# Optimization experiments

Measured on AMD Instinct MI355X. Metric: run time of the kernel, lower is better.

## Reference

```python
import math
import jax, jax.numpy as jnp
import numpy as np

INIT_TEMPERATURE = 0.07
MAX_SCALE = 100.0
B, D = 16384, 256


def setup_inputs() -> dict:
    key = jax.random.key(0)
    k1, k2 = jax.random.split(key)
    z_schema = jax.random.normal(k1, (B, D), dtype=jnp.float32)
    z_seal = jax.random.normal(k2, (B, D), dtype=jnp.float32)
    logit_scale = jnp.asarray(math.log(1.0 / INIT_TEMPERATURE), dtype=jnp.float32)
    return {"z_schema": z_schema, "z_seal": z_seal, "logit_scale": logit_scale}


def reference(z_schema, z_seal, logit_scale):
    # scale = min(exp(logit_scale), max_scale)
    scale = jnp.minimum(jnp.exp(logit_scale), jnp.float32(MAX_SCALE))
    # logits[i, j] = <z_schema[i], z_seal[j]> * scale   (B, B)
    logits = jnp.einsum("id,jd->ij", z_schema, z_seal) * scale
    # cross-entropy with labels = arange(B): loss = mean(lse(row) - diag)
    diag = jnp.diagonal(logits)
    lse_rows = jax.nn.logsumexp(logits, axis=1)  # s2r direction
    lse_cols = jax.nn.logsumexp(logits, axis=0)  # r2s direction (logits.T rows)
    loss_s2r = jnp.mean(lse_rows - diag)
    loss_r2s = jnp.mean(lse_cols - diag)
    loss = (loss_s2r + loss_r2s) * 0.5
    return (loss, loss)
```

## Files before the change

kernel.cpp:

```cpp
#include <hip/hip_runtime.h>
#include <hip/hip_bf16.h>
#include <math.h>

#define B_N 16384
#define D_K 256
#define JS 8
#define JRANGE (B_N / JS)
#define TJ 32
#define NT (JRANGE / TJ)
#define TILE_BYTES (TJ * D_K * 2)

typedef __bf16 bf16x8 __attribute__((ext_vector_type(8)));
typedef float f32x16 __attribute__((ext_vector_type(16)));

__device__ __forceinline__ unsigned short f2bf(float x) {
  unsigned u = __float_as_uint(x);
  unsigned r = (u + 0x7fffu + ((u >> 16) & 1u)) >> 16;
  return (unsigned short)r;
}

__device__ __forceinline__ float fexp2(float x) {
#if __has_builtin(__builtin_amdgcn_exp2f)
  return __builtin_amdgcn_exp2f(x);
#else
  return exp2f(x);
#endif
}

__device__ __forceinline__ void load_lds16(const void* g, void* l) {
  __builtin_amdgcn_global_load_lds(
      (const __attribute__((address_space(1))) unsigned int*)g,
      (__attribute__((address_space(3))) unsigned int*)l, 16, 0, 0);
}

__global__ void convert_kernel(const float* __restrict__ A, const float* __restrict__ Bm,
                               const float* __restrict__ lsp,
                               unsigned short* __restrict__ Abf,
                               unsigned short* __restrict__ Bbf) {
  const float c = fminf(expf(lsp[0]), 100.0f) * 1.4426950408889634f;
  int idx = (blockIdx.x * blockDim.x + threadIdx.x) * 4;
  float4 a = *(const float4*)(A + idx);
  float4 b = *(const float4*)(Bm + idx);
  ushort4 ua, ub;
  ua.x = f2bf(a.x); ua.y = f2bf(a.y); ua.z = f2bf(a.z); ua.w = f2bf(a.w);
  ub.x = f2bf(b.x * c); ub.y = f2bf(b.y * c); ub.z = f2bf(b.z * c); ub.w = f2bf(b.w * c);
  *(ushort4*)(Abf + idx) = ua;
  *(ushort4*)(Bbf + idx) = ub;
}

__global__ void diag_kernel(const float* __restrict__ A, const float* __restrict__ Bm,
                            float* __restrict__ diag) {
  int w = threadIdx.x >> 6, l = threadIdx.x & 63;
  int row = blockIdx.x * 4 + w;
  const float4* a = (const float4*)(A + row * D_K);
  const float4* b = (const float4*)(Bm + row * D_K);
  float4 av = a[l], bv = b[l];
  float s = av.x * bv.x + av.y * bv.y + av.z * bv.z + av.w * bv.w;
#pragma unroll
  for (int off = 32; off; off >>= 1) s += __shfl_xor(s, off);
  if (l == 0) diag[row] = s;
}

__device__ __forceinline__ void upd(float& m, float& s, const f32x16& a) {
  float t = a[0];
#pragma unroll
  for (int r = 1; r < 16; ++r) t = fmaxf(t, a[r]);
  float mn = fmaxf(m, t);
  s *= fexp2(m - mn);
  float p = 0.f;
#pragma unroll
  for (int r = 0; r < 16; ++r) p += fexp2(a[r] - mn);
  s += p;
  m = mn;
}

__global__ __launch_bounds__(256, 2) void lse_kernel(const unsigned short* __restrict__ Abf,
                                                     const unsigned short* __restrict__ Bbf,
                                                     float* __restrict__ pm,
                                                     float* __restrict__ ps) {
  __shared__ __align__(16) unsigned char lds[2][TILE_BYTES];
  const int bid = blockIdx.x;
  const int dir = bid >> 9;
  const int iblk = (bid >> 3) & 63;
  const int js = bid & 7;
  const unsigned short* X = dir ? Bbf : Abf;
  const unsigned short* Y = dir ? Abf : Bbf;
  const int i0 = iblk * 256;
  const int j0 = js * JRANGE;
  const int w = threadIdx.x >> 6;
  const int l = threadIdx.x & 63;
  const int lc = l & 31, lh = l >> 5;

  bf16x8 xf0[16], xf1[16];
  {
    const unsigned short* Xr0 = X + (size_t)(i0 + w * 64 + lc) * D_K + lh * 8;
    const unsigned short* Xr1 = Xr0 + 32 * D_K;
#pragma unroll
    for (int kk = 0; kk < 16; ++kk) {
      xf0[kk] = *(const bf16x8*)(Xr0 + kk * 16);
      xf1[kk] = *(const bf16x8*)(Xr1 + kk * 16);
    }
  }

  float m0 = -INFINITY, s0 = 0.f, m1 = -INFINITY, s1 = 0.f;

#define STAGE(bufidx, t)                                                        \
  {                                                                             \
    _Pragma("unroll") for (int r = 0; r < 4; ++r) {                             \
      const int row = w * 8 + 2 * r + lh;                                       \
      const unsigned short* src =                                               \
          Y + (size_t)(j0 + (t) * TJ + row) * D_K + ((lc ^ (2 * r + lh)) << 3); \
      load_lds16(src, &lds[bufidx][w * 4096 + r * 1024]);                       \
    }                                                                           \
  }

#define CONSUME(bufidx)                                                           \
  {                                                                              \
    f32x16 acc0 = {};                                                            \
    f32x16 acc1 = {};                                                            \
    _Pragma("unroll") for (int kk = 0; kk < 16; ++kk) {                          \
      bf16x8 y = *(const bf16x8*)(                                               \
          &lds[bufidx][lc * 512 + ((((kk << 1) | lh) ^ (lc & 7)) << 4)]);        \
      acc0 = __builtin_amdgcn_mfma_f32_32x32x16_bf16(y, xf0[kk], acc0, 0, 0, 0); \
      acc1 = __builtin_amdgcn_mfma_f32_32x32x16_bf16(y, xf1[kk], acc1, 0, 0, 0); \
    }                                                                            \
    upd(m0, s0, acc0);                                                           \
    upd(m1, s1, acc1);                                                           \
  }

  STAGE(0, 0);
  for (int t = 0; t < NT; t += 2) {
    __syncthreads();
    if (t + 1 < NT) STAGE(1, t + 1);
    CONSUME(0);
    __syncthreads();
    if (t + 2 < NT) STAGE(0, t + 2);
    CONSUME(1);
  }
#undef STAGE
#undef CONSUME

  {
    float mo = __shfl_xor(m0, 32), so = __shfl_xor(s0, 32);
    float mn = fmaxf(m0, mo);
    s0 = s0 * fexp2(m0 - mn) + so * fexp2(mo - mn); m0 = mn;
    mo = __shfl_xor(m1, 32); so = __shfl_xor(s1, 32);
    mn = fmaxf(m1, mo);
    s1 = s1 * fexp2(m1 - mn) + so * fexp2(mo - mn); m1 = mn;
  }

  if (lh == 0) {
    const int base = js * (2 * B_N) + dir * B_N + i0 + w * 64 + lc;
    pm[base] = m0;      ps[base] = s0;
    pm[base + 32] = m1; ps[base + 32] = s1;
  }
}

__global__ void combine_kernel(const float* __restrict__ pm, const float* __restrict__ ps,
                               float* __restrict__ lse) {
  int id = blockIdx.x * 256 + threadIdx.x;
  float m = -INFINITY, s = 0.f;
#pragma unroll
  for (int p = 0; p < JS; ++p) {
    float mo = pm[p * (2 * B_N) + id], so = ps[p * (2 * B_N) + id];
    float mn = fmaxf(m, mo);
    s = s * fexp2(m - mn) + so * fexp2(mo - mn);
    m = mn;
  }
  lse[id] = 0.6931471805599453f * (m + log2f(s));
}

__global__ void final_kernel(const float* __restrict__ lse, const float* __restrict__ diag,
                             const float* __restrict__ lsp, float* __restrict__ out) {
  const float scale = fminf(expf(lsp[0]), 100.0f);
  float part = 0.f;
  for (int i = threadIdx.x; i < B_N; i += 1024)
    part += 0.5f * (lse[i] + lse[B_N + i]) - scale * diag[i];
  __shared__ float red[1024];
  red[threadIdx.x] = part;
  __syncthreads();
  for (int off = 512; off; off >>= 1) {
    if (threadIdx.x < off) red[threadIdx.x] += red[threadIdx.x + off];
    __syncthreads();
  }
  if (threadIdx.x == 0) {
    float loss = red[0] / (float)B_N;
    out[0] = loss;
    out[1] = loss;
  }
}

extern "C" void kernel_launch(void* const* d_in, const int* in_sizes, int n_in,
                              void* d_out, int out_size, void* d_ws, size_t ws_size,
                              hipStream_t stream) {
  const float* A  = (const float*)d_in[0];
  const float* Bm = (const float*)d_in[1];
  const float* ls = (const float*)d_in[2];
  float* out = (float*)d_out;

  char* ws = (char*)d_ws;
  unsigned short* Abf = (unsigned short*)ws;
  unsigned short* Bbf = Abf + (size_t)B_N * D_K;
  float* diagp = (float*)(ws + 2ull * B_N * D_K * 2);
  float* lsep  = diagp + B_N;
  float* pm    = lsep + 2 * B_N;
  float* ps    = pm + JS * 2 * B_N;

  convert_kernel<<<4096, 256, 0, stream>>>(A, Bm, ls, Abf, Bbf);
  diag_kernel<<<4096, 256, 0, stream>>>(A, Bm, diagp);
  lse_kernel<<<1024, 256, 0, stream>>>(Abf, Bbf, pm, ps);
  combine_kernel<<<128, 256, 0, stream>>>(pm, ps, lsep);
  final_kernel<<<1, 1024, 0, stream>>>(lsep, diagp, ls, out);
}
```

Baseline: 332.6 us.

## Fuse diag into convert, raise lse occupancy, precompute load addresses, add MFMA priority

Computes the diagonal dot products inside the bf16 conversion kernel, which removes a launch and a second full read of both inputs. The LSE kernel raises its launch-bounds occupancy target from 2 to 4 blocks per CU, precomputes its global-to-LDS source pointers and the swizzled LDS read offset, and raises wave priority around the MFMA loop. The max and exp-sum reductions in the online softmax update are split into independent partial chains to expose more instruction-level parallelism. The higher occupancy target tightens the register budget, so register spilling is a risk given the 32 bf16x8 fragments held per thread.

```diff
diff --git a/kernel.cpp b/kernel.cpp
--- a/kernel.cpp
+++ b/kernel.cpp
@@ -33,12 +33,14 @@
       (__attribute__((address_space(3))) unsigned int*)l, 16, 0, 0);
 }
 
-__global__ void convert_kernel(const float* __restrict__ A, const float* __restrict__ Bm,
-                               const float* __restrict__ lsp,
-                               unsigned short* __restrict__ Abf,
-                               unsigned short* __restrict__ Bbf) {
+__global__ void convert_diag_kernel(const float* __restrict__ A, const float* __restrict__ Bm,
+                                    const float* __restrict__ lsp,
+                                    unsigned short* __restrict__ Abf,
+                                    unsigned short* __restrict__ Bbf,
+                                    float* __restrict__ diag) {
   const float c = fminf(expf(lsp[0]), 100.0f) * 1.4426950408889634f;
-  int idx = (blockIdx.x * blockDim.x + threadIdx.x) * 4;
+  const int tid = threadIdx.x;
+  const int idx = (blockIdx.x * 256 + tid) * 4;
   float4 a = *(const float4*)(A + idx);
   float4 b = *(const float4*)(Bm + idx);
   ushort4 ua, ub;
@@ -46,35 +48,35 @@
   ub.x = f2bf(b.x * c); ub.y = f2bf(b.y * c); ub.z = f2bf(b.z * c); ub.w = f2bf(b.w * c);
   *(ushort4*)(Abf + idx) = ua;
   *(ushort4*)(Bbf + idx) = ub;
-}
-
-__global__ void diag_kernel(const float* __restrict__ A, const float* __restrict__ Bm,
-                            float* __restrict__ diag) {
-  int w = threadIdx.x >> 6, l = threadIdx.x & 63;
-  int row = blockIdx.x * 4 + w;
-  const float4* a = (const float4*)(A + row * D_K);
-  const float4* b = (const float4*)(Bm + row * D_K);
-  float4 av = a[l], bv = b[l];
-  float s = av.x * bv.x + av.y * bv.y + av.z * bv.z + av.w * bv.w;
-#pragma unroll
-  for (int off = 32; off; off >>= 1) s += __shfl_xor(s, off);
-  if (l == 0) diag[row] = s;
+  float d = a.x * b.x + a.y * b.y + a.z * b.z + a.w * b.w;
+#pragma unroll
+  for (int off = 32; off; off >>= 1) d += __shfl_xor(d, off);
+  if ((tid & 63) == 0) diag[blockIdx.x * 4 + (tid >> 6)] = d;
 }
 
 __device__ __forceinline__ void upd(float& m, float& s, const f32x16& a) {
-  float t = a[0];
-#pragma unroll
-  for (int r = 1; r < 16; ++r) t = fmaxf(t, a[r]);
-  float mn = fmaxf(m, t);
+  float x0 = fmaxf(fmaxf(a[0], a[1]), a[2]);
+  float x1 = fmaxf(fmaxf(a[3], a[4]), a[5]);
+  float x2 = fmaxf(fmaxf(a[6], a[7]), a[8]);
+  float x3 = fmaxf(fmaxf(a[9], a[10]), a[11]);
+  float x4 = fmaxf(fmaxf(a[12], a[13]), a[14]);
+  float y0 = fmaxf(fmaxf(x0, x1), x2);
+  float y1 = fmaxf(fmaxf(x3, x4), a[15]);
+  float mn = fmaxf(m, fmaxf(y0, y1));
   s *= fexp2(m - mn);
-  float p = 0.f;
-#pragma unroll
-  for (int r = 0; r < 16; ++r) p += fexp2(a[r] - mn);
-  s += p;
+  float p0 = fexp2(a[0] - mn), p1 = fexp2(a[1] - mn);
+  float p2 = fexp2(a[2] - mn), p3 = fexp2(a[3] - mn);
+  p0 += fexp2(a[4] - mn);  p1 += fexp2(a[5] - mn);
+  p2 += fexp2(a[6] - mn);  p3 += fexp2(a[7] - mn);
+  p0 += fexp2(a[8] - mn);  p1 += fexp2(a[9] - mn);
+  p2 += fexp2(a[10] - mn); p3 += fexp2(a[11] - mn);
+  p0 += fexp2(a[12] - mn); p1 += fexp2(a[13] - mn);
+  p2 += fexp2(a[14] - mn); p3 += fexp2(a[15] - mn);
+  s += (p0 + p1) + (p2 + p3);
   m = mn;
 }
 
-__global__ __launch_bounds__(256, 2) void lse_kernel(const unsigned short* __restrict__ Abf,
+__global__ __launch_bounds__(256, 4) void lse_kernel(const unsigned short* __restrict__ Abf,
                                                      const unsigned short* __restrict__ Bbf,
                                                      float* __restrict__ pm,
                                                      float* __restrict__ ps) {
@@ -94,47 +96,57 @@
   bf16x8 xf0[16], xf1[16];
   {
     const unsigned short* Xr0 = X + (size_t)(i0 + w * 64 + lc) * D_K + lh * 8;
-    const unsigned short* Xr1 = Xr0 + 32 * D_K;
 #pragma unroll
     for (int kk = 0; kk < 16; ++kk) {
       xf0[kk] = *(const bf16x8*)(Xr0 + kk * 16);
-      xf1[kk] = *(const bf16x8*)(Xr1 + kk * 16);
+      xf1[kk] = *(const bf16x8*)(Xr0 + 32 * D_K + kk * 16);
     }
   }
 
   float m0 = -INFINITY, s0 = 0.f, m1 = -INFINITY, s1 = 0.f;
 
-#define STAGE(bufidx, t)                                                        \
+  const unsigned short* srcs[4];
+  unsigned dsts[4];
+#pragma unroll
+  for (int r = 0; r < 4; ++r) {
+    const int row = w * 8 + 2 * r + lh;
+    srcs[r] = Y + (size_t)(j0 + row) * D_K + ((lc ^ (row & 7)) << 3);
+    dsts[r] = w * 4096 + r * 1024;
+  }
+
+#define STAGE(bufidx)                                  \
+  {                                                    \
+    _Pragma("unroll") for (int r = 0; r < 4; ++r) {    \
+      load_lds16(srcs[r], &lds[bufidx][dsts[r]]);      \
+      srcs[r] += TJ * D_K;                             \
+    }                                                  \
+  }
+
+  const unsigned vb = (unsigned)lc * 512 + ((unsigned)(lh ^ (lc & 7)) << 4);
+
+#define CONSUME(bufidx)                                                          \
   {                                                                             \
-    _Pragma("unroll") for (int r = 0; r < 4; ++r) {                             \
-      const int row = w * 8 + 2 * r + lh;                                       \
-      const unsigned short* src =                                               \
-          Y + (size_t)(j0 + (t) * TJ + row) * D_K + ((lc ^ (2 * r + lh)) << 3); \
-      load_lds16(src, &lds[bufidx][w * 4096 + r * 1024]);                       \
+    f32x16 acc0 = {};                                                           \
+    f32x16 acc1 = {};                                                           \
+    const unsigned char* lb = &lds[bufidx][0];                                  \
+    __builtin_amdgcn_s_setprio(1);                                              \
+    _Pragma("unroll") for (int kk = 0; kk < 16; ++kk) {                         \
+      bf16x8 y = *(const bf16x8*)(lb + (vb ^ (unsigned)(kk << 5)));             \
+      acc0 = __builtin_amdgcn_mfma_f32_32x32x16_bf16(y, xf0[kk], acc0, 0, 0, 0);\
+      acc1 = __builtin_amdgcn_mfma_f32_32x32x16_bf16(y, xf1[kk], acc1, 0, 0, 0);\
     }                                                                           \
-  }
-
-#define CONSUME(bufidx)                                                           \
-  {                                                                              \
-    f32x16 acc0 = {};                                                            \
-    f32x16 acc1 = {};                                                            \
-    _Pragma("unroll") for (int kk = 0; kk < 16; ++kk) {                          \
-      bf16x8 y = *(const bf16x8*)(                                               \
-          &lds[bufidx][lc * 512 + ((((kk << 1) | lh) ^ (lc & 7)) << 4)]);        \
-      acc0 = __builtin_amdgcn_mfma_f32_32x32x16_bf16(y, xf0[kk], acc0, 0, 0, 0); \
-      acc1 = __builtin_amdgcn_mfma_f32_32x32x16_bf16(y, xf1[kk], acc1, 0, 0, 0); \
-    }                                                                            \
-    upd(m0, s0, acc0);                                                           \
-    upd(m1, s1, acc1);                                                           \
-  }
-
-  STAGE(0, 0);
+    __builtin_amdgcn_s_setprio(0);                                              \
+    upd(m0, s0, acc0);                                                          \
+    upd(m1, s1, acc1);                                                          \
+  }
+
+  STAGE(0);
   for (int t = 0; t < NT; t += 2) {
     __syncthreads();
-    if (t + 1 < NT) STAGE(1, t + 1);
+    if (t + 1 < NT) STAGE(1);
     CONSUME(0);
     __syncthreads();
-    if (t + 2 < NT) STAGE(0, t + 2);
+    if (t + 2 < NT) STAGE(0);
     CONSUME(1);
   }
 #undef STAGE
@@ -206,8 +218,7 @@
   float* pm    = lsep + 2 * B_N;
   float* ps    = pm + JS * 2 * B_N;
 
-  convert_kernel<<<4096, 256, 0, stream>>>(A, Bm, ls, Abf, Bbf);
-  diag_kernel<<<4096, 256, 0, stream>>>(A, Bm, diagp);
+  convert_diag_kernel<<<4096, 256, 0, stream>>>(A, Bm, ls, Abf, Bbf, diagp);
   lse_kernel<<<1024, 256, 0, stream>>>(Abf, Bbf, pm, ps);
   combine_kernel<<<128, 256, 0, stream>>>(pm, ps, lsep);
   final_kernel<<<1, 1024, 0, stream>>>(lsep, diagp, ls, out);
```

Measured after the change: 744.2 us. +123.7%, slower.
